# Kernel tuning notes

Measured on AMD Instinct MI355X. Metric: run time of the kernel, lower is better.

## Reference

```python
import jax, jax.numpy as jnp
import numpy as np

B, L = 2, 4096
D_MODEL = 1024
EXPAND = 2
D_INNER = EXPAND * D_MODEL            # 2048
HEADDIM = 64
NHEADS = D_INNER // HEADDIM           # 32
D_STATE = 128
NGROUPS = 1
D_CONV = 4
D_OUT = 1024
D_IN_PROJ = 2 * D_INNER + 2 * NGROUPS * D_STATE + NHEADS  # 4384
CONV_DIM = D_INNER + 2 * NGROUPS * D_STATE                # 2304
EPS = 1e-5


def setup_inputs() -> dict:
    key = jax.random.key(0)
    ks = jax.random.split(key, 8)
    x = jax.random.normal(ks[0], (B, L, D_MODEL), jnp.float32)
    in_proj_w = jax.random.normal(ks[1], (D_IN_PROJ, D_MODEL), jnp.float32) * (1.0 / np.sqrt(D_MODEL))
    conv_w = jax.random.normal(ks[2], (CONV_DIM, D_CONV), jnp.float32) * (1.0 / np.sqrt(D_CONV))
    conv_b = jnp.zeros((CONV_DIM,), jnp.float32)
    # dt_bias init as in the module: inverse-softplus of dt ~ LogUniform(1e-3, 1e-1)
    dt = jnp.exp(jax.random.uniform(ks[3], (NHEADS,)) * (np.log(0.1) - np.log(0.001)) + np.log(0.001))
    dt_bias = dt + jnp.log(-jnp.expm1(-dt))
    A_log = jnp.log(jax.random.uniform(ks[4], (NHEADS,), minval=1.0, maxval=16.0))
    Dp = jnp.ones((NHEADS,), jnp.float32)
    norm_w = jnp.ones((D_INNER,), jnp.float32)
    out_proj_w = jax.random.normal(ks[5], (D_OUT, D_INNER), jnp.float32) * (1.0 / np.sqrt(D_INNER))
    return {"x": x, "in_proj_w": in_proj_w, "conv_w": conv_w, "conv_b": conv_b,
            "dt_bias": dt_bias, "A_log": A_log, "Dp": Dp, "norm_w": norm_w,
            "out_proj_w": out_proj_w}


def _mamba_fwd(x, in_proj_w, conv_w, conv_b, dt_bias, A_log, Dp, norm_w, out_proj_w):
    # in_proj (no bias): (B,L,D_MODEL) -> (B,L,D_IN_PROJ)
    zxbcdt = jnp.einsum('bld,ed->ble', x, in_proj_w)
    z = zxbcdt[..., :D_INNER]                                  # gate branch
    xBC = zxbcdt[..., D_INNER:D_INNER + CONV_DIM]              # conv branch
    dt = zxbcdt[..., D_INNER + CONV_DIM:]                      # (B,L,H)
    # depthwise causal conv1d + SiLU
    xBC_t = jnp.transpose(xBC, (0, 2, 1))                      # (B, C, L)
    conv_out = jax.lax.conv_general_dilated(
        xBC_t, conv_w[:, None, :], window_strides=(1,),
        padding=[(D_CONV - 1, 0)],
        dimension_numbers=('NCH', 'OIH', 'NCH'),
        feature_group_count=CONV_DIM)
    xBC = jax.nn.silu(jnp.transpose(conv_out + conv_b[None, :, None], (0, 2, 1)))
    xs = xBC[..., :D_INNER].reshape(B, L, NHEADS, HEADDIM)     # (B,L,H,P)
    Bm = xBC[..., D_INNER:D_INNER + D_STATE]                   # (B,L,N), ngroups=1
    Cm = xBC[..., D_INNER + D_STATE:]                          # (B,L,N)
    A = -jnp.exp(A_log)                                        # (H,)
    dt = jax.nn.softplus(dt + dt_bias)                         # (B,L,H)
    dA = jnp.exp(dt * A)                                       # (B,L,H)

    def step(h, inp):
        dA_t, dt_t, B_t, x_t, C_t = inp
        # h: (B,H,P,N) selective state-space recurrence
        h = h * dA_t[:, :, None, None] + jnp.einsum('bh,bn,bhp->bhpn', dt_t, B_t, x_t)
        y = jnp.einsum('bhpn,bn->bhp', h, C_t)
        return h, y

    h0 = jnp.zeros((B, NHEADS, HEADDIM, D_STATE), xs.dtype)
    _, ys = jax.lax.scan(step, h0,
                         (jnp.swapaxes(dA, 0, 1), jnp.swapaxes(dt, 0, 1),
                          jnp.swapaxes(Bm, 0, 1), jnp.swapaxes(xs, 0, 1),
                          jnp.swapaxes(Cm, 0, 1)))
    y = jnp.swapaxes(ys, 0, 1) + Dp[None, None, :, None] * xs  # skip term D*x
    y = y.reshape(B, L, D_INNER)
    # gated RMSNorm (norm_before_gate=False): norm(y * silu(z)) * w
    y = y * jax.nn.silu(z)
    y = y * jax.lax.rsqrt(jnp.mean(y * y, axis=-1, keepdims=True) + EPS) * norm_w
    return jnp.einsum('bld,od->blo', y, out_proj_w)


def reference(x, in_proj_w, conv_w, conv_b, dt_bias, A_log, Dp, norm_w, out_proj_w):
    return _mamba_fwd(x, in_proj_w, conv_w, conv_b, dt_bias, A_log, Dp, norm_w, out_proj_w)
```

## Files before the change

kernel.cpp:

```cpp
#include <hip/hip_runtime.h>

#define LL 4096
#define DMODEL 1024
#define DINNER 2048
#define NHEADS 32
#define DSTATE 128
#define DINPROJ 4384
#define NZX 4352
#define CONVDIM 2304
#define ROWS 8192
#define Q 64
#define NCS 64
#define XCSEQ ((size_t)LL*CONVDIM)
#define LGSEQ ((size_t)NHEADS*NCS*Q)

typedef __attribute__((ext_vector_type(8))) __bf16 bf16x8;
typedef __attribute__((ext_vector_type(4))) float f32x4;

__device__ __forceinline__ float bf2f(ushort u){ union{uint i;float f;} v; v.i=(uint)u<<16; return v.f; }
__device__ __forceinline__ ushort f2bf(float f){ union{float f;uint i;} v; v.f=f; uint r=v.i+0x7fffu+((v.i>>16)&1u); return (ushort)(r>>16); }

__global__ __launch_bounds__(256) void cvt_k(const float4* __restrict__ src, uint4* __restrict__ dst){
  long t = (long)blockIdx.x*256 + threadIdx.x;
  float4 a = src[t*2], b = src[t*2+1];
  ushort u[8] = { f2bf(a.x),f2bf(a.y),f2bf(a.z),f2bf(a.w),
                  f2bf(b.x),f2bf(b.y),f2bf(b.z),f2bf(b.w) };
  dst[t] = *(uint4*)u;
}

__global__ __launch_bounds__(256) void padw_cvt(const float4* __restrict__ W, ushort4* __restrict__ Wp){
  int row = blockIdx.x, c = threadIdx.x;
  ushort4 o = make_ushort4(0,0,0,0);
  if (row < DINPROJ){
    float4 f = W[(size_t)row*256 + c];
    o = make_ushort4(f2bf(f.x), f2bf(f.y), f2bf(f.z), f2bf(f.w));
  }
  Wp[(size_t)row*256 + c] = o;
}

__device__ __forceinline__ void gld16(const void* g, void* l){
  __builtin_amdgcn_global_load_lds((const __attribute__((address_space(1))) void*)g,
                                   (__attribute__((address_space(3))) void*)l, 16, 0, 0);
}

#define GBM 128
#define GBN 128
#define GBK 32

__global__ __launch_bounds__(256) void gemm_tile(
    const ushort* __restrict__ A, int lda, long grow0, long rowmax,
    const ushort* __restrict__ W, int ldw,
    void* __restrict__ Cv, int ldc, int K, int obf, int swz, int q, int r,
    float* __restrict__ Cdt){
  __shared__ __align__(16) ushort As[2][GBM*GBK];
  __shared__ __align__(16) ushort Bs[2][GBN*GBK];
  const int tid = threadIdx.x;
  const int lane = tid & 63, wave = tid >> 6;
  const int wm = wave >> 1, wn = wave & 1;
  int bx, by;
  if (swz){
    int wgid = blockIdx.y * gridDim.x + blockIdx.x;
    int xcd = wgid & 7, i = wgid >> 3;
    int vid = (xcd < r) ? xcd*(q+1) + i : r*(q+1) + (xcd - r)*q + i;
    int rows = gridDim.y;
    if (((rows & 7) == 0) && (r == 0)){
      int rp = rows >> 3;
      int lv = vid - xcd*q;
      by = xcd*rp + (lv % rp);
      bx = lv / rp;
    } else { by = vid / (int)gridDim.x; bx = vid % (int)gridDim.x; }
  } else { bx = blockIdx.x; by = blockIdx.y; }
  const int m0 = by * GBM, n0 = bx * GBN;

  const int srow = lane >> 2;
  const int scol = (((lane & 3) ^ ((lane >> 3) & 3)) * 8);
  long ra0 = grow0 + m0 + 16*wave + srow;      if (ra0 < 0) ra0 = 0; if (ra0 > rowmax) ra0 = rowmax;
  long ra1 = grow0 + m0 + 64 + 16*wave + srow; if (ra1 < 0) ra1 = 0; if (ra1 > rowmax) ra1 = rowmax;
  const ushort* gA0 = A + ra0*(long)lda + scol;
  const ushort* gA1 = A + ra1*(long)lda + scol;
  const ushort* gB0 = W + (size_t)(n0 + 16*wave + srow)*ldw + scol;
  const ushort* gB1 = W + (size_t)(n0 + 64 + 16*wave + srow)*ldw + scol;
  ushort* lA0 = &As[0][0] + (16*wave)*GBK;
  ushort* lA1 = &As[0][0] + (64 + 16*wave)*GBK;
  ushort* lB0 = &Bs[0][0] + (16*wave)*GBK;
  ushort* lB1 = &Bs[0][0] + (64 + 16*wave)*GBK;

  const int fr = lane & 15, quad = lane >> 4;
  const int es = ((quad ^ ((fr >> 1) & 3)) * 8);
  f32x4 acc[4][4] = {};

#define STAGE(buf, ko) { \
    gld16(gA0 + (ko), lA0 + (buf)*(GBM*GBK)); \
    gld16(gA1 + (ko), lA1 + (buf)*(GBM*GBK)); \
    gld16(gB0 + (ko), lB0 + (buf)*(GBN*GBK)); \
    gld16(gB1 + (ko), lB1 + (buf)*(GBN*GBK)); }

  STAGE(0, 0);
  __syncthreads();
  int cur = 0;
  const int nst = K / GBK;
  for (int s = 0; s < nst; ++s){
    if (s + 1 < nst) STAGE(cur^1, (s+1)*GBK);
    const ushort* Ab = &As[cur][0];
    const ushort* Bb = &Bs[cur][0];
    bf16x8 af[4], bw[4];
    #pragma unroll
    for (int i=0;i<4;i++) af[i] = *(const bf16x8*)(Ab + (wm*64 + i*16 + fr)*GBK + es);
    #pragma unroll
    for (int j=0;j<4;j++) bw[j] = *(const bf16x8*)(Bb + (wn*64 + j*16 + fr)*GBK + es);
    #pragma unroll
    for (int i=0;i<4;i++)
      #pragma unroll
      for (int j=0;j<4;j++)
        acc[i][j] = __builtin_amdgcn_mfma_f32_16x16x32_bf16(af[i], bw[j], acc[i][j], 0,0,0);
    if (s + 1 < nst){ __syncthreads(); cur ^= 1; }
  }
#undef STAGE
  if (Cdt && n0 >= NZX){
    int nb = n0 - NZX;
    #pragma unroll
    for (int i=0;i<4;i++)
      #pragma unroll
      for (int j=0;j<4;j++){
        size_t base = (size_t)(m0 + wm*64 + i*16 + quad*4)*128 + (nb + wn*64 + j*16 + fr);
        #pragma unroll
        for (int rr=0;rr<4;rr++)
          Cdt[base + (size_t)rr*128] = acc[i][j][rr];
      }
  } else if (obf){
    ushort* Cb = (ushort*)Cv;
    #pragma unroll
    for (int i=0;i<4;i++)
      #pragma unroll
      for (int j=0;j<4;j++){
        size_t base = (size_t)(m0 + wm*64 + i*16 + quad*4)*ldc + (n0 + wn*64 + j*16 + fr);
        #pragma unroll
        for (int rr=0;rr<4;rr++)
          Cb[base + (size_t)rr*ldc] = f2bf(acc[i][j][rr]);
      }
  } else {
    float* Cf = (float*)Cv;
    #pragma unroll
    for (int i=0;i<4;i++)
      #pragma unroll
      for (int j=0;j<4;j++){
        size_t base = (size_t)(m0 + wm*64 + i*16 + quad*4)*ldc + (n0 + wn*64 + j*16 + fr);
        #pragma unroll
        for (int rr=0;rr<4;rr++)
          Cf[base + (size_t)rr*ldc] = acc[i][j][rr];
      }
  }
}

__global__ __launch_bounds__(256) void conv8(const ushort* __restrict__ zxh,
    const float* __restrict__ cw, const float* __restrict__ cb,
    ushort* __restrict__ xconv, int l0, long base){
  int z = blockIdx.y;
  long bb = base + (long)z*LL;
  ushort* xc = xconv + (size_t)z*XCSEQ;
  int id = blockIdx.x*256 + threadIdx.x;
  int g = id % 288, band = id / 288;
  int c = g*8;
  float w[8][4], bias[8];
  #pragma unroll
  for (int i=0;i<8;i++){
    bias[i] = cb[c+i];
    #pragma unroll
    for (int j=0;j<4;j++) w[i][j] = cw[(c+i)*4+j];
  }
  float in[7][8];
  #pragma unroll
  for (int k=0;k<7;k++){
    int lrow = l0 + band*4 - 3 + k;
    if (lrow < 0){
      #pragma unroll
      for (int i=0;i<8;i++) in[k][i] = 0.f;
    } else {
      uint4 v = *(const uint4*)(zxh + (size_t)(bb + band*4 - 3 + k)*NZX + DINNER + c);
      const ushort* us = (const ushort*)&v;
      #pragma unroll
      for (int i=0;i<8;i++) in[k][i] = bf2f(us[i]);
    }
  }
  #pragma unroll
  for (int r=0;r<4;r++){
    ushort o[8];
    #pragma unroll
    for (int i=0;i<8;i++){
      float a = bias[i];
      #pragma unroll
      for (int j=0;j<4;j++) a = fmaf(in[r+j][i], w[i][j], a);
      float v = a / (1.f + expf(-a));
      o[i] = f2bf(v);
    }
    *(uint4*)(xc + (size_t)(band*4 + r)*CONVDIM + c) = *(uint4*)o;
  }
}

__global__ __launch_bounds__(256) void scan_pre2(const ushort* __restrict__ xcv0,
    const float* __restrict__ dtraw, long dtrow0,
    const float* __restrict__ dtb, const float* __restrict__ alog,
    ushort* __restrict__ gbuf0, ushort* __restrict__ gbuf1,
    float* __restrict__ lgbuf0, int cslot0){
  const int c = blockIdx.x, h = blockIdx.y, z = blockIdx.z;
  const ushort* xcv = xcv0 + (size_t)z*XCSEQ;
  const long dtr0 = dtrow0 + (long)z*LL;
  ushort* gbuf = z ? gbuf1 : gbuf0;
  float* lgbuf = lgbuf0 + (size_t)z*LGSEQ;
  const int cslot = cslot0 + c;
  const int tid = threadIdx.x, lane = tid & 63, w = tid >> 6;
  const int l15 = lane & 15, quad = lane >> 4, kq = quad*8;
  __shared__ float wsx[Q];
  __shared__ __align__(16) ushort XT[64*72];
  __shared__ __align__(16) ushort BTw[128*72];
  const int c0 = c*Q;
  if (tid < 64){
    float xv = dtraw[(size_t)(dtr0 + c0 + tid)*128 + h] + dtb[h];
    float sp = (xv > 20.f) ? xv : log1pf(expf(xv));
    float la = sp * (-expf(alog[h]));
    float v = la;
    #pragma unroll
    for (int off=1; off<64; off<<=1){ float u = __shfl_up(v, off); if (tid >= off) v += u; }
    float tot = __shfl(v, 63);
    wsx[tid] = __expf(tot - v)*sp;
    lgbuf[((size_t)h*NCS + cslot)*Q + tid] = v;
  }
  __syncthreads();
  { int s = tid>>2, pb = (tid&3)*16;
    const ushort* src = xcv + (size_t)(c0+s)*CONVDIM + h*64 + pb;
    ushort tmp[16];
    *(uint4*)tmp     = *(const uint4*)src;
    *(uint4*)(tmp+8) = *(const uint4*)(src+8);
    #pragma unroll
    for (int i=0;i<16;i++) XT[(pb+i)*72 + s] = tmp[i];
  }
  { int s = tid>>2, nb4 = (tid&3)*32;
    const ushort* src = xcv + (size_t)(c0+s)*CONVDIM + DINNER + nb4;
    float wv = wsx[s];
    ushort tmp[32];
    #pragma unroll
    for (int v4=0;v4<4;v4++) *(uint4*)(tmp+v4*8) = *(const uint4*)(src+v4*8);
    #pragma unroll
    for (int i=0;i<32;i++) BTw[(nb4+i)*72 + s] = f2bf(bf2f(tmp[i])*wv);
  }
  __syncthreads();
  f32x4 g[8] = {};
  #pragma unroll
  for (int kb=0;kb<2;kb++){
    bf16x8 afr = *(const bf16x8*)(XT + (16*w + l15)*72 + kb*32 + kq);
    #pragma unroll
    for (int j=0;j<8;j++){
      bf16x8 bfr = *(const bf16x8*)(BTw + (16*j + l15)*72 + kb*32 + kq);
      g[j] = __builtin_amdgcn_mfma_f32_16x16x32_bf16(afr, bfr, g[j], 0,0,0);
    }
  }
  __syncthreads();
  ushort* gst = &BTw[0];
  #pragma unroll
  for (int j=0;j<8;j++)
    #pragma unroll
    for (int r=0;r<4;r++)
      gst[(16*w + quad*4 + r)*136 + 16*j + l15] = f2bf(g[j][r]);
  __syncthreads();
  { int row = tid >> 2, seg = tid & 3;
    const ushort* gs = gst + row*136 + seg*32;
    uint4 a = *(const uint4*)(gs);
    uint4 b = *(const uint4*)(gs + 8);
    uint4 c2 = *(const uint4*)(gs + 16);
    uint4 d = *(const uint4*)(gs + 24);
    ushort* gdst = gbuf + ((size_t)h*NCS + cslot)*8192 + row*128 + seg*32;
    *(uint4*)gdst = a;
    *(uint4*)(gdst + 8) = b;
    *(uint4*)(gdst + 16) = c2;
    *(uint4*)(gdst + 24) = d;
  }
}

__global__ __launch_bounds__(256) void scan_carry2(ushort* __restrict__ g0p,
    ushort* __restrict__ g1p, const float* __restrict__ lgbuf0, int ncs){
  const int qtr = blockIdx.x, h = blockIdx.y, z = blockIdx.z;
  ushort* gh = z ? g1p : g0p;
  const float* lgbuf = lgbuf0 + (size_t)z*LGSEQ;
  const int tid = threadIdx.x;
  __shared__ float es[NCS];
  if (tid < ncs) es[tid] = __expf(lgbuf[((size_t)h*NCS + tid)*Q + 63]);
  __syncthreads();
  float hreg[8] = {0.f,0.f,0.f,0.f,0.f,0.f,0.f,0.f};
  ushort* p0 = gh + (size_t)h*NCS*8192 + qtr*2048 + tid*8;
  uint4 g0 = *(const uint4*)p0;
  uint4 g1 = *(const uint4*)(p0 + 8192);
  for (int c = 0; c < ncs; ++c){
    ushort* pc = p0 + (size_t)c*8192;
    uint4 gc = g0; g0 = g1;
    if (c + 2 < ncs) g1 = *(const uint4*)(pc + 2*8192);
    ushort u[8];
    #pragma unroll
    for (int i=0;i<8;i++) u[i] = f2bf(hreg[i]);
    *(uint4*)pc = *(uint4*)u;
    float e = es[c];
    const ushort* gs = (const ushort*)&gc;
    #pragma unroll
    for (int i=0;i<8;i++) hreg[i] = fmaf(hreg[i], e, bf2f(gs[i]));
  }
}

__global__ __launch_bounds__(256) void scan_y2(ushort* __restrict__ xcv0,
    const float* __restrict__ dtraw, long dtrow0,
    const float* __restrict__ dtb, const float* __restrict__ alog,
    const float* __restrict__ lgbuf0, const ushort* __restrict__ gbuf0,
    const ushort* __restrict__ gbuf1, const float* __restrict__ Dp, int cslot0){
  const int c = blockIdx.x, h = blockIdx.y, z = blockIdx.z;
  ushort* xcv = xcv0 + (size_t)z*XCSEQ;
  const long dtr0 = dtrow0 + (long)z*LL;
  const ushort* gbuf = z ? gbuf1 : gbuf0;
  const float* lgbuf = lgbuf0 + (size_t)z*LGSEQ;
  const int cslot = cslot0 + c;
  const int tid = threadIdx.x, lane = tid & 63, w = tid >> 6;
  const int l15 = lane & 15, quad = lane >> 4, kq = quad*8;
  __shared__ float lg[Q], dts[Q], els[Q];
  __shared__ __align__(16) ushort XT[64*72];
  __shared__ __align__(16) ushort Ps[64*72];
  const int c0 = c*Q;
  if (tid < 64){
    float v = lgbuf[((size_t)h*NCS + cslot)*Q + tid];
    lg[tid] = v;
    els[tid] = __expf(v);
    float xv = dtraw[(size_t)(dtr0 + c0 + tid)*128 + h] + dtb[h];
    dts[tid] = (xv > 20.f) ? xv : log1pf(expf(xv));
  }
  { int s = tid>>2, pb = (tid&3)*16;
    const ushort* src = xcv + (size_t)(c0+s)*CONVDIM + h*64 + pb;
    ushort tmp[16];
    *(uint4*)tmp     = *(const uint4*)src;
    *(uint4*)(tmp+8) = *(const uint4*)(src+8);
    #pragma unroll
    for (int i=0;i<16;i++) XT[(pb+i)*72 + s] = tmp[i];
  }
  __syncthreads();
  {
    const ushort* Crow = xcv + (size_t)(c0 + 16*w + l15)*CONVDIM + DINNER + DSTATE;
    f32x4 sac[4] = {};
    #pragma unroll
    for (int kb=0;kb<4;kb++){
      bf16x8 afr = *(const bf16x8*)(Crow + kb*32 + kq);
      #pragma unroll
      for (int j=0;j<4;j++){
        const ushort* Brow = xcv + (size_t)(c0 + 16*j + l15)*CONVDIM + DINNER;
        bf16x8 bfr = *(const bf16x8*)(Brow + kb*32 + kq);
        sac[j] = __builtin_amdgcn_mfma_f32_16x16x32_bf16(afr, bfr, sac[j], 0,0,0);
      }
    }
    #pragma unroll
    for (int j=0;j<4;j++){
      int s = 16*j + l15;
      float lgs = lg[s], dtss = dts[s];
      #pragma unroll
      for (int r=0;r<4;r++){
        int t = 16*w + quad*4 + r;
        float val = (t >= s) ? sac[j][r]*__expf(lg[t]-lgs)*dtss : 0.f;
        Ps[t*72 + s] = f2bf(val);
      }
    }
  }
  __syncthreads();
  float yv[4][4];
  {
    const float dph = Dp[h];
    bf16x8 hb[4], xb[2];
    const ushort* hrow = gbuf + ((size_t)h*NCS + cslot)*8192 + (16*w + l15)*128;
    #pragma unroll
    for (int kb=0;kb<4;kb++) hb[kb] = *(const bf16x8*)(hrow + kb*32 + kq);
    #pragma unroll
    for (int kb=0;kb<2;kb++) xb[kb] = *(const bf16x8*)(XT + (16*w + l15)*72 + kb*32 + kq);
    #pragma unroll
    for (int i=0;i<4;i++){
      const ushort* Crow = xcv + (size_t)(c0 + 16*i + l15)*CONVDIM + DINNER + DSTATE;
      f32x4 y2 = {};
      #pragma unroll
      for (int kb=0;kb<4;kb++){
        bf16x8 afr = *(const bf16x8*)(Crow + kb*32 + kq);
        y2 = __builtin_amdgcn_mfma_f32_16x16x32_bf16(afr, hb[kb], y2, 0,0,0);
      }
      f32x4 y1 = {};
      #pragma unroll
      for (int kb=0;kb<2;kb++){
        bf16x8 afr = *(const bf16x8*)(Ps + (16*i + l15)*72 + kb*32 + kq);
        y1 = __builtin_amdgcn_mfma_f32_16x16x32_bf16(afr, xb[kb], y1, 0,0,0);
      }
      int p = 16*w + l15;
      #pragma unroll
      for (int r=0;r<4;r++){
        int t = 16*i + quad*4 + r;
        float xv = bf2f(XT[p*72 + t]);
        yv[i][r] = y1[r] + els[t]*y2[r] + dph*xv;
      }
    }
  }
  __syncthreads();
  {
    int p = 16*w + l15;
    #pragma unroll
    for (int i=0;i<4;i++)
      #pragma unroll
      for (int r=0;r<4;r++)
        Ps[(16*i + quad*4 + r)*72 + p] = f2bf(yv[i][r]);
  }
  __syncthreads();
  { int t = tid >> 2, seg = tid & 3;
    uint4 a = *(const uint4*)(Ps + t*72 + seg*16);
    uint4 b = *(const uint4*)(Ps + t*72 + seg*16 + 8);
    ushort* od = xcv + (size_t)(c0 + t)*CONVDIM + h*64 + seg*16;
    *(uint4*)od = a;
    *(uint4*)(od + 8) = b;
  }
}

__global__ __launch_bounds__(256) void gate_norm2(const ushort* __restrict__ ybase0,
    const ushort* __restrict__ zbase0, ushort* __restrict__ obase0,
    const float* __restrict__ nw){
  int lr = blockIdx.x, z = blockIdx.y, tid = threadIdx.x;
  const ushort* ybase = ybase0 + (size_t)z*XCSEQ;
  const ushort* zbase = zbase0 + (size_t)z*LL*NZX;
  ushort* obase = obase0 + (size_t)z*LL*NZX;
  int d0 = tid*8;
  const ushort* yrow = ybase + (size_t)lr*CONVDIM;
  const ushort* zrow = zbase + (size_t)lr*NZX;
  uint4 yu = *(const uint4*)(yrow + d0);
  uint4 zu = *(const uint4*)(zrow + d0);
  const ushort* yus = (const ushort*)&yu;
  const ushort* zus = (const ushort*)&zu;
  float y[8]; float ss = 0.f;
  #pragma unroll
  for (int i=0;i<8;i++){
    float zz = bf2f(zus[i]);
    float g = zz / (1.f + expf(-zz));
    float v = bf2f(yus[i]) * g;
    y[i] = v; ss += v*v;
  }
  #pragma unroll
  for (int m=1;m<64;m<<=1) ss += __shfl_xor(ss, m);
  __shared__ float red[4];
  if ((tid & 63) == 0) red[tid>>6] = ss;
  __syncthreads();
  ss = red[0]+red[1]+red[2]+red[3];
  float scale = rsqrtf(ss * (1.f/DINNER) + 1e-5f);
  ushort o[8];
  #pragma unroll
  for (int i=0;i<8;i++)
    o[i] = f2bf(y[i] * scale * nw[d0+i]);
  *(uint4*)(obase + (size_t)lr*NZX + d0) = *(uint4*)o;
}

extern "C" void kernel_launch(void* const* d_in, const int* in_sizes, int n_in,
                              void* d_out, int out_size, void* d_ws, size_t ws_size,
                              hipStream_t stream) {
  const float* x    = (const float*)d_in[0];
  const float* ipw  = (const float*)d_in[1];
  const float* cw   = (const float*)d_in[2];
  const float* cb   = (const float*)d_in[3];
  const float* dtb  = (const float*)d_in[4];
  const float* alog = (const float*)d_in[5];
  const float* Dp   = (const float*)d_in[6];
  const float* nw   = (const float*)d_in[7];
  const float* opw  = (const float*)d_in[8];
  char* ws = (char*)d_ws;
  size_t off = 0;
  ushort* Wp    = (ushort*)(ws + off); off += (size_t)4480*DMODEL*2;
  ushort* opwb  = (ushort*)(ws + off); off += (size_t)DMODEL*DINNER*2;
  float*  dtraw = (float*)(ws + off);  off += (size_t)ROWS*128*4;
  ushort* zxbh  = (ushort*)(ws + off); off += (size_t)ROWS*NZX*2;

  const size_t lg_b  = LGSEQ*4;
  const size_t xc_b  = XCSEQ*2;
  const size_t xc_fb = (size_t)1024*CONVDIM*2;
  const size_t gb_b  = (size_t)NHEADS*NCS*8192*2;

  size_t needA = off + 2*lg_b + 2*xc_b + gb_b;
  size_t needB = off + lg_b + xc_b + gb_b;
  int mode = (ws_size >= needA) ? 2 : (ws_size >= needB ? 1 : 0);

  float* lgbuf = (float*)(ws + off); off += (mode == 2) ? 2*lg_b : lg_b;
  ushort* xconv = (ushort*)(ws + off);
  off += (mode == 2) ? 2*xc_b : (mode == 1 ? xc_b : xc_fb);
  ushort* xbf  = (ushort*)(ws + off);
  ushort* gbuf0 = (ushort*)(ws + off);
  ushort* gbuf1 = (mode == 2) ? (ushort*)d_out : gbuf0;

  cvt_k<<<ROWS*DMODEL/8/256, 256, 0, stream>>>((const float4*)x, (uint4*)xbf);
  padw_cvt<<<4480, 256, 0, stream>>>((const float4*)ipw, (ushort4*)Wp);
  cvt_k<<<DMODEL*DINNER/8/256, 256, 0, stream>>>((const float4*)opw, (uint4*)opwb);

  gemm_tile<<<dim3(35, 64), 256, 0, stream>>>(
      xbf, DMODEL, 0, (long)ROWS-1, Wp, DMODEL,
      zxbh, NZX, DMODEL, 1, 1, 280, 0, dtraw);

  if (mode == 2){
    conv8<<<dim3(288*(LL/4)/256, 2), 256, 0, stream>>>(zxbh, cw, cb, xconv, 0, 0);
    scan_pre2<<<dim3(NCS, NHEADS, 2), 256, 0, stream>>>(
        xconv, dtraw, 0, dtb, alog, gbuf0, gbuf1, lgbuf, 0);
    scan_carry2<<<dim3(4, NHEADS, 2), 256, 0, stream>>>(gbuf0, gbuf1, lgbuf, NCS);
    scan_y2<<<dim3(NCS, NHEADS, 2), 256, 0, stream>>>(
        xconv, dtraw, 0, dtb, alog, lgbuf, gbuf0, gbuf1, Dp, 0);
    gate_norm2<<<dim3(LL, 2), 256, 0, stream>>>(xconv, zxbh, zxbh + DINNER, nw);
  } else if (mode == 1){
    for (int b = 0; b < 2; ++b){
      long row0 = (long)b*LL;
      conv8<<<dim3(288*(LL/4)/256, 1), 256, 0, stream>>>(zxbh, cw, cb, xconv, 0, row0);
      scan_pre2<<<dim3(NCS, NHEADS, 1), 256, 0, stream>>>(
          xconv, dtraw, row0, dtb, alog, gbuf0, gbuf0, lgbuf, 0);
      scan_carry2<<<dim3(4, NHEADS, 1), 256, 0, stream>>>(gbuf0, gbuf0, lgbuf, NCS);
      scan_y2<<<dim3(NCS, NHEADS, 1), 256, 0, stream>>>(
          xconv, dtraw, row0, dtb, alog, lgbuf, gbuf0, gbuf0, Dp, 0);
      gate_norm2<<<dim3(LL, 1), 256, 0, stream>>>(
          xconv, zxbh + (size_t)row0*NZX, zxbh + (size_t)row0*NZX + DINNER, nw);
    }
  } else {
    for (int b = 0; b < 2; ++b){
      long row0 = (long)b*LL;
      for (int ckl = 0; ckl < 4; ++ckl){
        long g0 = row0 + (long)ckl*1024;
        conv8<<<dim3(288*(1024/4)/256, 1), 256, 0, stream>>>(zxbh, cw, cb, xconv, ckl*1024, g0);
        scan_pre2<<<dim3(16, NHEADS, 1), 256, 0, stream>>>(
            xconv, dtraw, g0, dtb, alog, gbuf0, gbuf0, lgbuf, ckl*16);
      }
      scan_carry2<<<dim3(4, NHEADS, 1), 256, 0, stream>>>(gbuf0, gbuf0, lgbuf, NCS);
      for (int ckl = 0; ckl < 4; ++ckl){
        long g0 = row0 + (long)ckl*1024;
        conv8<<<dim3(288*(1024/4)/256, 1), 256, 0, stream>>>(zxbh, cw, cb, xconv, ckl*1024, g0);
        scan_y2<<<dim3(16, NHEADS, 1), 256, 0, stream>>>(
            xconv, dtraw, g0, dtb, alog, lgbuf, gbuf0, gbuf0, Dp, ckl*16);
        gate_norm2<<<dim3(1024, 1), 256, 0, stream>>>(
            xconv, zxbh + (size_t)g0*NZX, zxbh + (size_t)g0*NZX + DINNER, nw);
      }
    }
  }

  gemm_tile<<<dim3(8, 64), 256, 0, stream>>>(
      zxbh + DINNER, NZX, 0, (long)ROWS-1, opwb, DINNER,
      (float*)d_out, DMODEL, DINNER, 0, 1, 64, 0, nullptr);
}
```

Baseline: 442.0 us.

## Fuse causal conv into scan kernels and merge conversion launches

Removes the standalone conv8 kernel. Both scan_pre2 and scan_y2 now recompute the depthwise causal conv plus SiLU directly from the in_proj output rows into shared memory. scan_y2 stages B and C in LDS instead of reading them from global memory, and writes y to a separate buffer. The three fp32-to-bf16 conversion kernels are merged into one launch. This avoids writing and re-reading the conv output, at the cost of computing the conv redundantly: once per head for the B/C channels and once in each of the two scan passes.

```diff
diff --git a/kernel.cpp b/kernel.cpp
--- a/kernel.cpp
+++ b/kernel.cpp
@@ -20,22 +20,32 @@
 __device__ __forceinline__ float bf2f(ushort u){ union{uint i;float f;} v; v.i=(uint)u<<16; return v.f; }
 __device__ __forceinline__ ushort f2bf(float f){ union{float f;uint i;} v; v.f=f; uint r=v.i+0x7fffu+((v.i>>16)&1u); return (ushort)(r>>16); }
 
-__global__ __launch_bounds__(256) void cvt_k(const float4* __restrict__ src, uint4* __restrict__ dst){
-  long t = (long)blockIdx.x*256 + threadIdx.x;
-  float4 a = src[t*2], b = src[t*2+1];
-  ushort u[8] = { f2bf(a.x),f2bf(a.y),f2bf(a.z),f2bf(a.w),
-                  f2bf(b.x),f2bf(b.y),f2bf(b.z),f2bf(b.w) };
-  dst[t] = *(uint4*)u;
-}
-
-__global__ __launch_bounds__(256) void padw_cvt(const float4* __restrict__ W, ushort4* __restrict__ Wp){
-  int row = blockIdx.x, c = threadIdx.x;
-  ushort4 o = make_ushort4(0,0,0,0);
-  if (row < DINPROJ){
-    float4 f = W[(size_t)row*256 + c];
-    o = make_ushort4(f2bf(f.x), f2bf(f.y), f2bf(f.z), f2bf(f.w));
-  }
-  Wp[(size_t)row*256 + c] = o;
+__global__ __launch_bounds__(256) void cvt_all(
+    const float4* __restrict__ x, uint4* __restrict__ xbf,
+    const float4* __restrict__ ipw, ushort4* __restrict__ Wp,
+    const float4* __restrict__ opw, uint4* __restrict__ opwb){
+  int b = blockIdx.x, tid = threadIdx.x;
+  if (b < 4096){
+    long t = (long)b*256 + tid;
+    float4 a = x[t*2], bb = x[t*2+1];
+    ushort u[8] = { f2bf(a.x),f2bf(a.y),f2bf(a.z),f2bf(a.w),
+                    f2bf(bb.x),f2bf(bb.y),f2bf(bb.z),f2bf(bb.w) };
+    xbf[t] = *(uint4*)u;
+  } else if (b < 4096 + 4480){
+    int row = b - 4096;
+    ushort4 o = make_ushort4(0,0,0,0);
+    if (row < DINPROJ){
+      float4 f = ipw[(size_t)row*256 + tid];
+      o = make_ushort4(f2bf(f.x), f2bf(f.y), f2bf(f.z), f2bf(f.w));
+    }
+    Wp[(size_t)row*256 + tid] = o;
+  } else {
+    long t = (long)(b - 8576)*256 + tid;
+    float4 a = opw[t*2], bb = opw[t*2+1];
+    ushort u[8] = { f2bf(a.x),f2bf(a.y),f2bf(a.z),f2bf(a.w),
+                    f2bf(bb.x),f2bf(bb.y),f2bf(bb.z),f2bf(bb.w) };
+    opwb[t] = *(uint4*)u;
+  }
 }
 
 __device__ __forceinline__ void gld16(const void* g, void* l){
@@ -152,59 +162,43 @@
   }
 }
 
-__global__ __launch_bounds__(256) void conv8(const ushort* __restrict__ zxh,
+__device__ __forceinline__ void conv16(const uint4 rv[4][2],
     const float* __restrict__ cw, const float* __restrict__ cb,
-    ushort* __restrict__ xconv, int l0, long base){
-  int z = blockIdx.y;
-  long bb = base + (long)z*LL;
-  ushort* xc = xconv + (size_t)z*XCSEQ;
-  int id = blockIdx.x*256 + threadIdx.x;
-  int g = id % 288, band = id / 288;
-  int c = g*8;
-  float w[8][4], bias[8];
-  #pragma unroll
-  for (int i=0;i<8;i++){
-    bias[i] = cb[c+i];
-    #pragma unroll
-    for (int j=0;j<4;j++) w[i][j] = cw[(c+i)*4+j];
-  }
-  float in[7][8];
-  #pragma unroll
-  for (int k=0;k<7;k++){
-    int lrow = l0 + band*4 - 3 + k;
-    if (lrow < 0){
-      #pragma unroll
-      for (int i=0;i<8;i++) in[k][i] = 0.f;
-    } else {
-      uint4 v = *(const uint4*)(zxh + (size_t)(bb + band*4 - 3 + k)*NZX + DINNER + c);
-      const ushort* us = (const ushort*)&v;
-      #pragma unroll
-      for (int i=0;i<8;i++) in[k][i] = bf2f(us[i]);
-    }
-  }
-  #pragma unroll
-  for (int r=0;r<4;r++){
-    ushort o[8];
-    #pragma unroll
-    for (int i=0;i<8;i++){
-      float a = bias[i];
-      #pragma unroll
-      for (int j=0;j<4;j++) a = fmaf(in[r+j][i], w[i][j], a);
-      float v = a / (1.f + expf(-a));
-      o[i] = f2bf(v);
-    }
-    *(uint4*)(xc + (size_t)(band*4 + r)*CONVDIM + c) = *(uint4*)o;
-  }
-}
-
-__global__ __launch_bounds__(256) void scan_pre2(const ushort* __restrict__ xcv0,
-    const float* __restrict__ dtraw, long dtrow0,
+    int ch0, float out[16]){
+  #pragma unroll
+  for (int i=0;i<16;i++){
+    int ch = ch0 + i;
+    float4 cwv = *(const float4*)(cw + ch*4);
+    float a = cb[ch];
+    #pragma unroll
+    for (int j=0;j<4;j++){
+      const ushort* us = (const ushort*)&rv[j][0];
+      a = fmaf(bf2f(us[i]), (&cwv.x)[j], a);
+    }
+    out[i] = a / (1.f + expf(-a));
+  }
+}
+
+__device__ __forceinline__ void ldrows(const ushort* __restrict__ rbase, int l,
+    uint4 rv[4][2]){
+  #pragma unroll
+  for (int j=0;j<4;j++){
+    if (l - 3 + j >= 0){
+      rv[j][0] = *(const uint4*)(rbase + (size_t)j*NZX);
+      rv[j][1] = *(const uint4*)(rbase + (size_t)j*NZX + 8);
+    } else { rv[j][0] = make_uint4(0,0,0,0); rv[j][1] = make_uint4(0,0,0,0); }
+  }
+}
+
+__global__ __launch_bounds__(256) void scan_pre2(const ushort* __restrict__ zxh,
+    long grow0, int l0off,
+    const float* __restrict__ dtraw,
+    const float* __restrict__ cw, const float* __restrict__ cb,
     const float* __restrict__ dtb, const float* __restrict__ alog,
     ushort* __restrict__ gbuf0, ushort* __restrict__ gbuf1,
     float* __restrict__ lgbuf0, int cslot0){
   const int c = blockIdx.x, h = blockIdx.y, z = blockIdx.z;
-  const ushort* xcv = xcv0 + (size_t)z*XCSEQ;
-  const long dtr0 = dtrow0 + (long)z*LL;
+  const long grow = grow0 + (long)z*LL;
   ushort* gbuf = z ? gbuf1 : gbuf0;
   float* lgbuf = lgbuf0 + (size_t)z*LGSEQ;
   const int cslot = cslot0 + c;
@@ -215,7 +209,7 @@
   __shared__ __align__(16) ushort BTw[128*72];
   const int c0 = c*Q;
   if (tid < 64){
-    float xv = dtraw[(size_t)(dtr0 + c0 + tid)*128 + h] + dtb[h];
+    float xv = dtraw[(size_t)(grow + c0 + tid)*128 + h] + dtb[h];
     float sp = (xv > 20.f) ? xv : log1pf(expf(xv));
     float la = sp * (-expf(alog[h]));
     float v = la;
@@ -225,23 +219,29 @@
     wsx[tid] = __expf(tot - v)*sp;
     lgbuf[((size_t)h*NCS + cslot)*Q + tid] = v;
   }
-  __syncthreads();
-  { int s = tid>>2, pb = (tid&3)*16;
-    const ushort* src = xcv + (size_t)(c0+s)*CONVDIM + h*64 + pb;
-    ushort tmp[16];
-    *(uint4*)tmp     = *(const uint4*)src;
-    *(uint4*)(tmp+8) = *(const uint4*)(src+8);
-    #pragma unroll
-    for (int i=0;i<16;i++) XT[(pb+i)*72 + s] = tmp[i];
-  }
-  { int s = tid>>2, nb4 = (tid&3)*32;
-    const ushort* src = xcv + (size_t)(c0+s)*CONVDIM + DINNER + nb4;
-    float wv = wsx[s];
-    ushort tmp[32];
-    #pragma unroll
-    for (int v4=0;v4<4;v4++) *(uint4*)(tmp+v4*8) = *(const uint4*)(src+v4*8);
-    #pragma unroll
-    for (int i=0;i<32;i++) BTw[(nb4+i)*72 + s] = f2bf(bf2f(tmp[i])*wv);
+  const int s = tid>>2;
+  const int l = l0off + c0 + s;
+  const ushort* rowb = zxh + (size_t)(grow + c0 + s - 3)*NZX + DINNER;
+  { int pb = (tid&3)*16;
+    uint4 rv[4][2];
+    ldrows(rowb + h*64 + pb, l, rv);
+    float o[16];
+    conv16(rv, cw, cb, h*64 + pb, o);
+    #pragma unroll
+    for (int i=0;i<16;i++) XT[(pb+i)*72 + s] = f2bf(o[i]);
+  }
+  __syncthreads();
+  { float wv = wsx[s];
+    #pragma unroll
+    for (int half=0; half<2; half++){
+      int cc = (tid&3)*32 + half*16;
+      uint4 rv[4][2];
+      ldrows(rowb + 2048 + cc, l, rv);
+      float o[16];
+      conv16(rv, cw, cb, 2048 + cc, o);
+      #pragma unroll
+      for (int i=0;i<16;i++) BTw[(cc+i)*72 + s] = f2bf(o[i]*wv);
+    }
   }
   __syncthreads();
   f32x4 g[8] = {};
@@ -304,62 +304,80 @@
   }
 }
 
-__global__ __launch_bounds__(256) void scan_y2(ushort* __restrict__ xcv0,
-    const float* __restrict__ dtraw, long dtrow0,
+__global__ __launch_bounds__(256) void scan_y2(const ushort* __restrict__ zxh,
+    long grow0, int l0off,
+    const float* __restrict__ dtraw,
+    const float* __restrict__ cw, const float* __restrict__ cb,
     const float* __restrict__ dtb, const float* __restrict__ alog,
     const float* __restrict__ lgbuf0, const ushort* __restrict__ gbuf0,
-    const ushort* __restrict__ gbuf1, const float* __restrict__ Dp, int cslot0){
+    const ushort* __restrict__ gbuf1, const float* __restrict__ Dp,
+    ushort* __restrict__ yb0, int cslot0){
   const int c = blockIdx.x, h = blockIdx.y, z = blockIdx.z;
-  ushort* xcv = xcv0 + (size_t)z*XCSEQ;
-  const long dtr0 = dtrow0 + (long)z*LL;
+  const long grow = grow0 + (long)z*LL;
   const ushort* gbuf = z ? gbuf1 : gbuf0;
   const float* lgbuf = lgbuf0 + (size_t)z*LGSEQ;
+  ushort* yb = yb0 + (size_t)z*XCSEQ;
   const int cslot = cslot0 + c;
   const int tid = threadIdx.x, lane = tid & 63, w = tid >> 6;
   const int l15 = lane & 15, quad = lane >> 4, kq = quad*8;
   __shared__ float lg[Q], dts[Q], els[Q];
   __shared__ __align__(16) ushort XT[64*72];
-  __shared__ __align__(16) ushort Ps[64*72];
+  __shared__ __align__(16) ushort Cc[64*136];
+  __shared__ __align__(16) ushort BP[64*136];
   const int c0 = c*Q;
   if (tid < 64){
     float v = lgbuf[((size_t)h*NCS + cslot)*Q + tid];
     lg[tid] = v;
     els[tid] = __expf(v);
-    float xv = dtraw[(size_t)(dtr0 + c0 + tid)*128 + h] + dtb[h];
+    float xv = dtraw[(size_t)(grow + c0 + tid)*128 + h] + dtb[h];
     dts[tid] = (xv > 20.f) ? xv : log1pf(expf(xv));
   }
-  { int s = tid>>2, pb = (tid&3)*16;
-    const ushort* src = xcv + (size_t)(c0+s)*CONVDIM + h*64 + pb;
-    ushort tmp[16];
-    *(uint4*)tmp     = *(const uint4*)src;
-    *(uint4*)(tmp+8) = *(const uint4*)(src+8);
-    #pragma unroll
-    for (int i=0;i<16;i++) XT[(pb+i)*72 + s] = tmp[i];
-  }
-  __syncthreads();
-  {
-    const ushort* Crow = xcv + (size_t)(c0 + 16*w + l15)*CONVDIM + DINNER + DSTATE;
-    f32x4 sac[4] = {};
-    #pragma unroll
-    for (int kb=0;kb<4;kb++){
-      bf16x8 afr = *(const bf16x8*)(Crow + kb*32 + kq);
-      #pragma unroll
-      for (int j=0;j<4;j++){
-        const ushort* Brow = xcv + (size_t)(c0 + 16*j + l15)*CONVDIM + DINNER;
-        bf16x8 bfr = *(const bf16x8*)(Brow + kb*32 + kq);
-        sac[j] = __builtin_amdgcn_mfma_f32_16x16x32_bf16(afr, bfr, sac[j], 0,0,0);
-      }
-    }
+  const int s = tid>>2;
+  const int l = l0off + c0 + s;
+  const ushort* rowb = zxh + (size_t)(grow + c0 + s - 3)*NZX + DINNER;
+  { int pb = (tid&3)*16;
+    uint4 rv[4][2];
+    ldrows(rowb + h*64 + pb, l, rv);
+    float o[16];
+    conv16(rv, cw, cb, h*64 + pb, o);
+    #pragma unroll
+    for (int i=0;i<16;i++) XT[(pb+i)*72 + s] = f2bf(o[i]);
+  }
+  #pragma unroll
+  for (int half=0; half<2; half++){
+    int cc = (tid&3)*32 + half*16;
+    uint4 rv[4][2];
+    float o[16];
+    ldrows(rowb + 2048 + cc, l, rv);
+    conv16(rv, cw, cb, 2048 + cc, o);
+    #pragma unroll
+    for (int i=0;i<16;i++) BP[s*136 + cc + i] = f2bf(o[i]);
+    ldrows(rowb + 2176 + cc, l, rv);
+    conv16(rv, cw, cb, 2176 + cc, o);
+    #pragma unroll
+    for (int i=0;i<16;i++) Cc[s*136 + cc + i] = f2bf(o[i]);
+  }
+  __syncthreads();
+  f32x4 sac[4] = {};
+  #pragma unroll
+  for (int kb=0;kb<4;kb++){
+    bf16x8 afr = *(const bf16x8*)(Cc + (16*w + l15)*136 + kb*32 + kq);
     #pragma unroll
     for (int j=0;j<4;j++){
-      int s = 16*j + l15;
-      float lgs = lg[s], dtss = dts[s];
-      #pragma unroll
-      for (int r=0;r<4;r++){
-        int t = 16*w + quad*4 + r;
-        float val = (t >= s) ? sac[j][r]*__expf(lg[t]-lgs)*dtss : 0.f;
-        Ps[t*72 + s] = f2bf(val);
-      }
+      bf16x8 bfr = *(const bf16x8*)(BP + (16*j + l15)*136 + kb*32 + kq);
+      sac[j] = __builtin_amdgcn_mfma_f32_16x16x32_bf16(afr, bfr, sac[j], 0,0,0);
+    }
+  }
+  __syncthreads();
+  #pragma unroll
+  for (int j=0;j<4;j++){
+    int ss = 16*j + l15;
+    float lgs = lg[ss], dtss = dts[ss];
+    #pragma unroll
+    for (int r=0;r<4;r++){
+      int t = 16*w + quad*4 + r;
+      float val = (t >= ss) ? sac[j][r]*__expf(lg[t]-lgs)*dtss : 0.f;
+      BP[t*72 + ss] = f2bf(val);
     }
   }
   __syncthreads();
@@ -374,17 +392,16 @@
     for (int kb=0;kb<2;kb++) xb[kb] = *(const bf16x8*)(XT + (16*w + l15)*72 + kb*32 + kq);
     #pragma unroll
     for (int i=0;i<4;i++){
-      const ushort* Crow = xcv + (size_t)(c0 + 16*i + l15)*CONVDIM + DINNER + DSTATE;
       f32x4 y2 = {};
       #pragma unroll
       for (int kb=0;kb<4;kb++){
-        bf16x8 afr = *(const bf16x8*)(Crow + kb*32 + kq);
+        bf16x8 afr = *(const bf16x8*)(Cc + (16*i + l15)*136 + kb*32 + kq);
         y2 = __builtin_amdgcn_mfma_f32_16x16x32_bf16(afr, hb[kb], y2, 0,0,0);
       }
       f32x4 y1 = {};
       #pragma unroll
       for (int kb=0;kb<2;kb++){
-        bf16x8 afr = *(const bf16x8*)(Ps + (16*i + l15)*72 + kb*32 + kq);
+        bf16x8 afr = *(const bf16x8*)(BP + (16*i + l15)*72 + kb*32 + kq);
         y1 = __builtin_amdgcn_mfma_f32_16x16x32_bf16(afr, xb[kb], y1, 0,0,0);
       }
       int p = 16*w + l15;
@@ -403,13 +420,13 @@
     for (int i=0;i<4;i++)
       #pragma unroll
       for (int r=0;r<4;r++)
-        Ps[(16*i + quad*4 + r)*72 + p] = f2bf(yv[i][r]);
+        BP[(16*i + quad*4 + r)*72 + p] = f2bf(yv[i][r]);
   }
   __syncthreads();
   { int t = tid >> 2, seg = tid & 3;
-    uint4 a = *(const uint4*)(Ps + t*72 + seg*16);
-    uint4 b = *(const uint4*)(Ps + t*72 + seg*16 + 8);
-    ushort* od = xcv + (size_t)(c0 + t)*CONVDIM + h*64 + seg*16;
+    uint4 a = *(const uint4*)(BP + t*72 + seg*16);
+    uint4 b = *(const uint4*)(BP + t*72 + seg*16 + 8);
+    ushort* od = yb + (size_t)(c0 + t)*CONVDIM + h*64 + seg*16;
     *(uint4*)od = a;
     *(uint4*)(od + 8) = b;
   }
@@ -471,66 +488,62 @@
   ushort* zxbh  = (ushort*)(ws + off); off += (size_t)ROWS*NZX*2;
 
   const size_t lg_b  = LGSEQ*4;
-  const size_t xc_b  = XCSEQ*2;
-  const size_t xc_fb = (size_t)1024*CONVDIM*2;
+  const size_t yb_b  = XCSEQ*2;
+  const size_t yb_fb = (size_t)1024*CONVDIM*2;
   const size_t gb_b  = (size_t)NHEADS*NCS*8192*2;
 
-  size_t needA = off + 2*lg_b + 2*xc_b + gb_b;
-  size_t needB = off + lg_b + xc_b + gb_b;
+  size_t needA = off + 2*lg_b + 2*yb_b + gb_b;
+  size_t needB = off + lg_b + yb_b + gb_b;
   int mode = (ws_size >= needA) ? 2 : (ws_size >= needB ? 1 : 0);
 
   float* lgbuf = (float*)(ws + off); off += (mode == 2) ? 2*lg_b : lg_b;
-  ushort* xconv = (ushort*)(ws + off);
-  off += (mode == 2) ? 2*xc_b : (mode == 1 ? xc_b : xc_fb);
+  ushort* ybuf = (ushort*)(ws + off);
+  off += (mode == 2) ? 2*yb_b : (mode == 1 ? yb_b : yb_fb);
   ushort* xbf  = (ushort*)(ws + off);
   ushort* gbuf0 = (ushort*)(ws + off);
   ushort* gbuf1 = (mode == 2) ? (ushort*)d_out : gbuf0;
 
-  cvt_k<<<ROWS*DMODEL/8/256, 256, 0, stream>>>((const float4*)x, (uint4*)xbf);
-  padw_cvt<<<4480, 256, 0, stream>>>((const float4*)ipw, (ushort4*)Wp);
-  cvt_k<<<DMODEL*DINNER/8/256, 256, 0, stream>>>((const float4*)opw, (uint4*)opwb);
+  cvt_all<<<9600, 256, 0, stream>>>((const float4*)x, (uint4*)xbf,
+                                    (const float4*)ipw, (ushort4*)Wp,
+                                    (const float4*)opw, (uint4*)opwb);
 
   gemm_tile<<<dim3(35, 64), 256, 0, stream>>>(
       xbf, DMODEL, 0, (long)ROWS-1, Wp, DMODEL,
       zxbh, NZX, DMODEL, 1, 1, 280, 0, dtraw);
 
   if (mode == 2){
-    conv8<<<dim3(288*(LL/4)/256, 2), 256, 0, stream>>>(zxbh, cw, cb, xconv, 0, 0);
     scan_pre2<<<dim3(NCS, NHEADS, 2), 256, 0, stream>>>(
-        xconv, dtraw, 0, dtb, alog, gbuf0, gbuf1, lgbuf, 0);
+        zxbh, 0, 0, dtraw, cw, cb, dtb, alog, gbuf0, gbuf1, lgbuf, 0);
     scan_carry2<<<dim3(4, NHEADS, 2), 256, 0, stream>>>(gbuf0, gbuf1, lgbuf, NCS);
     scan_y2<<<dim3(NCS, NHEADS, 2), 256, 0, stream>>>(
-        xconv, dtraw, 0, dtb, alog, lgbuf, gbuf0, gbuf1, Dp, 0);
-    gate_norm2<<<dim3(LL, 2), 256, 0, stream>>>(xconv, zxbh, zxbh + DINNER, nw);
+        zxbh, 0, 0, dtraw, cw, cb, dtb, alog, lgbuf, gbuf0, gbuf1, Dp, ybuf, 0);
+    gate_norm2<<<dim3(LL, 2), 256, 0, stream>>>(ybuf, zxbh, zxbh + DINNER, nw);
   } else if (mode == 1){
     for (int b = 0; b < 2; ++b){
       long row0 = (long)b*LL;
-      conv8<<<dim3(288*(LL/4)/256, 1), 256, 0, stream>>>(zxbh, cw, cb, xconv, 0, row0);
       scan_pre2<<<dim3(NCS, NHEADS, 1), 256, 0, stream>>>(
-          xconv, dtraw, row0, dtb, alog, gbuf0, gbuf0, lgbuf, 0);
+          zxbh, row0, 0, dtraw, cw, cb, dtb, alog, gbuf0, gbuf0, lgbuf, 0);
       scan_carry2<<<dim3(4, NHEADS, 1), 256, 0, stream>>>(gbuf0, gbuf0, lgbuf, NCS);
       scan_y2<<<dim3(NCS, NHEADS, 1), 256, 0, stream>>>(
-          xconv, dtraw, row0, dtb, alog, lgbuf, gbuf0, gbuf0, Dp, 0);
+          zxbh, row0, 0, dtraw, cw, cb, dtb, alog, lgbuf, gbuf0, gbuf0, Dp, ybuf, 0);
       gate_norm2<<<dim3(LL, 1), 256, 0, stream>>>(
-          xconv, zxbh + (size_t)row0*NZX, zxbh + (size_t)row0*NZX + DINNER, nw);
+          ybuf, zxbh + (size_t)row0*NZX, zxbh + (size_t)row0*NZX + DINNER, nw);
     }
   } else {
     for (int b = 0; b < 2; ++b){
       long row0 = (long)b*LL;
       for (int ckl = 0; ckl < 4; ++ckl){
         long g0 = row0 + (long)ckl*1024;
-        conv8<<<dim3(288*(1024/4)/256, 1), 256, 0, stream>>>(zxbh, cw, cb, xconv, ckl*1024, g0);
         scan_pre2<<<dim3(16, NHEADS, 1), 256, 0, stream>>>(
-            xconv, dtraw, g0, dtb, alog, gbuf0, gbuf0, lgbuf, ckl*16);
+            zxbh, g0, ckl*1024, dtraw, cw, cb, dtb, alog, gbuf0, gbuf0, lgbuf, ckl*16);
       }
       scan_carry2<<<dim3(4, NHEADS, 1), 256, 0, stream>>>(gbuf0, gbuf0, lgbuf, NCS);
       for (int ckl = 0; ckl < 4; ++ckl){
         long g0 = row0 + (long)ckl*1024;
-        conv8<<<dim3(288*(1024/4)/256, 1), 256, 0, stream>>>(zxbh, cw, cb, xconv, ckl*1024, g0);
         scan_y2<<<dim3(16, NHEADS, 1), 256, 0, stream>>>(
-            xconv, dtraw, g0, dtb, alog, lgbuf, gbuf0, gbuf0, Dp, ckl*16);
+            zxbh, g0, ckl*1024, dtraw, cw, cb, dtb, alog, lgbuf, gbuf0, gbuf0, Dp, ybuf, ckl*16);
         gate_norm2<<<dim3(1024, 1), 256, 0, stream>>>(
-            xconv, zxbh + (size_t)g0*NZX, zxbh + (size_t)g0*NZX + DINNER, nw);
+            ybuf, zxbh + (size_t)g0*NZX, zxbh + (size_t)g0*NZX + DINNER, nw);
       }
     }
   }
```

After: 675.2 us. 1.53x slower.
